# Optimization experiments

Hardware: AMD Instinct MI355X
Metric: run time of the kernel (lower is better)

The kernel has to match this reference:

```python
import jax, jax.numpy as jnp
import numpy as np

B, S, D, H = 8, 8192, 256, 256


def setup_inputs() -> dict:
    key = jax.random.key(0)
    ks = jax.random.split(key, 5)
    scale = 1.0 / np.sqrt(D)  # mimic nn.Linear init scale
    return {
        "x": jax.random.normal(ks[0], (B, S, D), dtype=jnp.float32),
        "h0": jnp.zeros((B, 1, H), dtype=jnp.float32),
        "w_h_w": jax.random.normal(ks[1], (H, D), dtype=jnp.float32) * scale,
        "w_h_b": jax.random.normal(ks[2], (H,), dtype=jnp.float32) * scale,
        "w_z_w": jax.random.normal(ks[3], (H, D), dtype=jnp.float32) * scale,
        "w_z_b": jax.random.normal(ks[4], (H,), dtype=jnp.float32) * scale,
    }


def reference(x, h0, w_h_w, w_h_b, w_z_w, w_z_b):
    # Projections over the whole sequence (same math as per-step Linear calls)
    z = jax.nn.sigmoid(jnp.einsum('bsd,hd->bsh', x, w_z_w) + w_z_b)  # [B,S,H]
    h_tilde = jnp.einsum('bsd,hd->bsh', x, w_h_w) + w_h_b            # [B,S,H]

    def step(h_prev, zh):
        z_t, ht_t = zh  # each [B,H]
        h_t = (1.0 - z_t) * h_prev + z_t * ht_t
        return h_t, h_t

    # scan over time axis; carry is [B,H]
    _, hs = jax.lax.scan(step, h0[:, 0],
                         (jnp.swapaxes(z, 0, 1), jnp.swapaxes(h_tilde, 0, 1)))
    return jnp.swapaxes(hs, 0, 1)  # [B,S,H]
```

## Files before the change

### kernel.cpp

```cpp
#include <hip/hip_runtime.h>
#include <math.h>


constexpr int B_ = 8;
constexpr int S_ = 8192;
constexpr int D_ = 256;
constexpr int H_ = 256;
constexpr int M_ = B_ * S_;
constexpr int CHUNKS = 128;
constexpr int CLEN = S_ / CHUNKS;

typedef __attribute__((ext_vector_type(8))) short bf16x8;
typedef __attribute__((ext_vector_type(4))) float f32x4;

__device__ __forceinline__ uint pack2bf(float f0, float f1) {
  const uint u0 = __float_as_uint(f0) + 0x8000u;
  const uint u1 = __float_as_uint(f1) + 0x8000u;
  return __builtin_amdgcn_perm(u1, u0, 0x07060302u);
}

__device__ __forceinline__ float a_of(uint u) { return __uint_as_float(u << 16); }
__device__ __forceinline__ float b_of(uint u) { return __uint_as_float(u & 0xFFFF0000u); }

__global__ __launch_bounds__(256) void gemm_zh(
    const float* __restrict__ x,
    const float* __restrict__ whw, const float* __restrict__ whb,
    const float* __restrict__ wzw, const float* __restrict__ wzb,
    uint* __restrict__ ab, float2* __restrict__ chunkPQ)
{
  __shared__ ushort xs[128][72];
  __shared__ ushort wzs[64][72];
  __shared__ ushort whs[64][72];

  const int tid = threadIdx.x;
  const int g    = blockIdx.x;
  const int xcd  = g & 7;
  const int loc  = g >> 3;
  const int nt   = loc & 3;
  const int panel = (loc >> 2) * 8 + xcd;
  const int m0 = panel * 128;
  const int n0 = nt * 64;

  const int lane = tid & 63;
  const int w  = tid >> 6;
  const int mb = (w & 1) * 64;
  const int nb = (w >> 1) * 32;
  const int q  = lane >> 4;
  const int cn = lane & 15;

  f32x4 accz[4][2] = {};
  f32x4 acch[4][2] = {};

  for (int k0 = 0; k0 < D_; k0 += 64) {
    __syncthreads();
#pragma unroll
    for (int f = 0; f < 8; f++) {
      const int idx = tid + 256 * f;
      const int row = idx >> 4, seg = idx & 15;
      float4 v = *(const float4*)(x + (size_t)(m0 + row) * D_ + k0 + seg * 4);
      *(uint2*)&xs[row][seg * 4] =
          make_uint2(pack2bf(v.x, v.y), pack2bf(v.z, v.w));
    }
#pragma unroll
    for (int f = 0; f < 4; f++) {
      const int idx = tid + 256 * f;
      const int row = idx >> 4, seg = idx & 15;
      float4 vz = *(const float4*)(wzw + (size_t)(n0 + row) * D_ + k0 + seg * 4);
      float4 vh = *(const float4*)(whw + (size_t)(n0 + row) * D_ + k0 + seg * 4);
      *(uint2*)&wzs[row][seg * 4] =
          make_uint2(pack2bf(vz.x, vz.y), pack2bf(vz.z, vz.w));
      *(uint2*)&whs[row][seg * 4] =
          make_uint2(pack2bf(vh.x, vh.y), pack2bf(vh.z, vh.w));
    }
    __syncthreads();
#pragma unroll
    for (int ks = 0; ks < 2; ks++) {
      const int kk = ks * 32 + q * 8;
      bf16x8 af[4], bz[2], bh[2];
#pragma unroll
      for (int i = 0; i < 4; i++)
        af[i] = *(const bf16x8*)&xs[mb + i * 16 + cn][kk];
#pragma unroll
      for (int j = 0; j < 2; j++) {
        bz[j] = *(const bf16x8*)&wzs[nb + j * 16 + cn][kk];
        bh[j] = *(const bf16x8*)&whs[nb + j * 16 + cn][kk];
      }
#pragma unroll
      for (int i = 0; i < 4; i++)
#pragma unroll
        for (int j = 0; j < 2; j++) {
          accz[i][j] = __builtin_amdgcn_mfma_f32_16x16x32_bf16(af[i], bz[j], accz[i][j], 0, 0, 0);
          acch[i][j] = __builtin_amdgcn_mfma_f32_16x16x32_bf16(af[i], bh[j], acch[i][j], 0, 0, 0);
        }
    }
  }

  const int row0 = m0 + mb;
  const int bb2  = row0 >> 13;
  const int cc   = (row0 & 8191) >> 6;

#pragma unroll
  for (int j = 0; j < 2; j++) {
    const int ch = n0 + nb + j * 16 + cn;
    const float zb = wzb[ch], hb = whb[ch];
    uint u[4][4];
#pragma unroll
    for (int i = 0; i < 4; i++) {
#pragma unroll
      for (int r = 0; r < 4; r++) {
        const int row = m0 + mb + i * 16 + q * 4 + r;
        const float zpre = accz[i][j][r] + zb;
        const float hpre = acch[i][j][r] + hb;
        const float e = __expf(-zpre);
        const float rcp = __builtin_amdgcn_rcpf(1.0f + e);
        const uint pk = pack2bf(e * rcp, hpre * rcp);
        ab[(size_t)row * H_ + ch] = pk;
        u[i][r] = pk;
      }
    }
    float P[4], Q[4];
#pragma unroll
    for (int i = 0; i < 4; i++) {
      float Pi = 1.f, Qi = 0.f;
#pragma unroll
      for (int r = 0; r < 4; r++) {
        const float a  = a_of(u[i][r]);
        const float bv = b_of(u[i][r]);
        Qi = fmaf(a, Qi, bv);
        Pi *= a;
      }
      P[i] = Pi; Q[i] = Qi;
    }
#pragma unroll
    for (int i = 0; i < 4; i++) {
      {
        const float Pp = __shfl_xor(P[i], 16);
        const float Qp = __shfl_xor(Q[i], 16);
        const bool later = (lane & 16) != 0;
        Q[i] = later ? fmaf(P[i], Qp, Q[i]) : fmaf(Pp, Q[i], Qp);
        P[i] = P[i] * Pp;
      }
      {
        const float Pp = __shfl_xor(P[i], 32);
        const float Qp = __shfl_xor(Q[i], 32);
        const bool later = (lane & 32) != 0;
        Q[i] = later ? fmaf(P[i], Qp, Q[i]) : fmaf(Pp, Q[i], Qp);
        P[i] = P[i] * Pp;
      }
    }
    float Pc = P[0], Qc = Q[0];
#pragma unroll
    for (int i = 1; i < 4; i++) {
      Qc = fmaf(P[i], Qc, Q[i]);
      Pc *= P[i];
    }
    if (lane < 16)
      chunkPQ[((size_t)bb2 * CHUNKS + cc) * H_ + ch] = make_float2(Pc, Qc);
  }
}

__global__ __launch_bounds__(256) void scan_phaseB(
    const float* __restrict__ h0in, const float2* __restrict__ pq,
    float* __restrict__ hstate)
{
  const int b = blockIdx.x;
  const int h = threadIdx.x;
  const size_t base = (size_t)b * CHUNKS * H_ + h;
  float hc = h0in[(size_t)b * H_ + h];
  for (int c0 = 0; c0 < CHUNKS; c0 += 16) {
    float2 v[16];
#pragma unroll
    for (int j = 0; j < 16; j++)
      v[j] = pq[base + (size_t)(c0 + j) * H_];
#pragma unroll
    for (int j = 0; j < 16; j++) {
      hstate[base + (size_t)(c0 + j) * H_] = hc;
      hc = fmaf(v[j].x, hc, v[j].y);
    }
  }
}

__global__ __launch_bounds__(256) void scan_phaseC(
    const uint* __restrict__ ab, const float* __restrict__ hstate,
    float* __restrict__ out)
{
  const int cid = blockIdx.x * 4 + (threadIdx.x >> 6);
  const int b = cid >> 7;
  const int c = cid & (CHUNKS - 1);
  const int ch4 = (threadIdx.x & 63) * 4;
  const size_t ebase = ((size_t)b * S_ + (size_t)c * CLEN) * H_ + ch4;

  float4 h4 = *(const float4*)(hstate + ((size_t)b * CHUNKS + c) * H_ + ch4);
  float h0v = h4.x, h1v = h4.y, h2v = h4.z, h3v = h4.w;

#pragma unroll
  for (int t0 = 0; t0 < CLEN; t0 += 8) {
    uint4 v[8];
#pragma unroll
    for (int j = 0; j < 8; j++)
      v[j] = *(const uint4*)(ab + ebase + (size_t)(t0 + j) * H_);
#pragma unroll
    for (int j = 0; j < 8; j++) {
      float4 o;
      o.x = h0v = fmaf(a_of(v[j].x), h0v, b_of(v[j].x));
      o.y = h1v = fmaf(a_of(v[j].y), h1v, b_of(v[j].y));
      o.z = h2v = fmaf(a_of(v[j].z), h2v, b_of(v[j].z));
      o.w = h3v = fmaf(a_of(v[j].w), h3v, b_of(v[j].w));
      *(float4*)(out + ebase + (size_t)(t0 + j) * H_) = o;
    }
  }
}

extern "C" void kernel_launch(void* const* d_in, const int* in_sizes, int n_in,
                              void* d_out, int out_size, void* d_ws, size_t ws_size,
                              hipStream_t stream) {
  const float* x   = (const float*)d_in[0];
  const float* h0  = (const float*)d_in[1];
  const float* whw = (const float*)d_in[2];
  const float* whb = (const float*)d_in[3];
  const float* wzw = (const float*)d_in[4];
  const float* wzb = (const float*)d_in[5];
  float* out = (float*)d_out;

  uint*   ab      = (uint*)d_ws;
  float2* chunkPQ = (float2*)(ab + (size_t)M_ * H_);
  float*  hstate  = (float*)(chunkPQ + (size_t)B_ * CHUNKS * H_);

  gemm_zh<<<(M_ / 128) * 4, 256, 0, stream>>>(x, whw, whb, wzw, wzb, ab, chunkPQ);
  scan_phaseB<<<B_, 256, 0, stream>>>(h0, (const float2*)chunkPQ, hstate);
  scan_phaseC<<<(B_ * CHUNKS) / 4, 256, 0, stream>>>(ab, hstate, out);
}
```

Measured before the change: 185.2 us.

## Pre-convert weights to bf16 once and widen GEMM tile to 128 columns

Adds a small prep kernel that converts both weight matrices to bf16 once, so the GEMM loads packed bf16 weights with 16-byte loads instead of converting fp32 weights in every block. The GEMM block grows to 512 threads covering a 128x128 output tile, halving the number of times each x panel is read and converted. The scan phase C is relaunched as one 64-thread block per chunk. This costs an extra kernel launch and more shared memory per block, which may reduce occupancy.

After: 177.2 us. 4.3% less time.

```diff
diff --git a/kernel.cpp b/kernel.cpp
--- a/kernel.cpp
+++ b/kernel.cpp
@@ -22,24 +22,34 @@
 __device__ __forceinline__ float a_of(uint u) { return __uint_as_float(u << 16); }
 __device__ __forceinline__ float b_of(uint u) { return __uint_as_float(u & 0xFFFF0000u); }
 
-__global__ __launch_bounds__(256) void gemm_zh(
-    const float* __restrict__ x,
-    const float* __restrict__ whw, const float* __restrict__ whb,
-    const float* __restrict__ wzw, const float* __restrict__ wzb,
+__global__ __launch_bounds__(256) void prep_w(
+    const float* __restrict__ wzw, const float* __restrict__ whw,
+    uint4* __restrict__ wb)
+{
+  const int u = blockIdx.x * 256 + threadIdx.x;
+  const int proj = u >> 13;
+  const float* s = (proj ? whw : wzw) + (size_t)(u & 8191) * 8;
+  wb[u] = make_uint4(pack2bf(s[0], s[1]), pack2bf(s[2], s[3]),
+                     pack2bf(s[4], s[5]), pack2bf(s[6], s[7]));
+}
+
+__global__ __launch_bounds__(512, 4) void gemm_zh(
+    const float* __restrict__ x, const ushort* __restrict__ wbu,
+    const float* __restrict__ whb, const float* __restrict__ wzb,
     uint* __restrict__ ab, float2* __restrict__ chunkPQ)
 {
   __shared__ ushort xs[128][72];
-  __shared__ ushort wzs[64][72];
-  __shared__ ushort whs[64][72];
+  __shared__ ushort wzs[128][72];
+  __shared__ ushort whs[128][72];
 
   const int tid = threadIdx.x;
   const int g    = blockIdx.x;
   const int xcd  = g & 7;
   const int loc  = g >> 3;
-  const int nt   = loc & 3;
-  const int panel = (loc >> 2) * 8 + xcd;
+  const int nt   = loc & 1;
+  const int panel = (loc >> 1) * 8 + xcd;
   const int m0 = panel * 128;
-  const int n0 = nt * 64;
+  const int n0 = nt * 128;
 
   const int lane = tid & 63;
   const int w  = tid >> 6;
@@ -54,8 +64,8 @@
   for (int k0 = 0; k0 < D_; k0 += 64) {
     __syncthreads();
 #pragma unroll
-    for (int f = 0; f < 8; f++) {
-      const int idx = tid + 256 * f;
+    for (int f = 0; f < 4; f++) {
+      const int idx = tid + 512 * f;
       const int row = idx >> 4, seg = idx & 15;
       float4 v = *(const float4*)(x + (size_t)(m0 + row) * D_ + k0 + seg * 4);
       *(uint2*)&xs[row][seg * 4] =
@@ -63,14 +73,13 @@
     }
 #pragma unroll
     for (int f = 0; f < 4; f++) {
-      const int idx = tid + 256 * f;
-      const int row = idx >> 4, seg = idx & 15;
-      float4 vz = *(const float4*)(wzw + (size_t)(n0 + row) * D_ + k0 + seg * 4);
-      float4 vh = *(const float4*)(whw + (size_t)(n0 + row) * D_ + k0 + seg * 4);
-      *(uint2*)&wzs[row][seg * 4] =
-          make_uint2(pack2bf(vz.x, vz.y), pack2bf(vz.z, vz.w));
-      *(uint2*)&whs[row][seg * 4] =
-          make_uint2(pack2bf(vh.x, vh.y), pack2bf(vh.z, vh.w));
+      const int idx = tid + 512 * f;
+      const int proj = idx >> 10;
+      const int r   = (idx >> 3) & 127, seg = idx & 7;
+      const uint4 v = *(const uint4*)(wbu + (size_t)proj * H_ * D_ +
+                                      (size_t)(n0 + r) * D_ + k0 + seg * 8);
+      ushort* dst = proj ? &whs[r][seg * 8] : &wzs[r][seg * 8];
+      *(uint4*)dst = v;
     }
     __syncthreads();
 #pragma unroll
@@ -180,14 +189,14 @@
   }
 }
 
-__global__ __launch_bounds__(256) void scan_phaseC(
+__global__ __launch_bounds__(64) void scan_phaseC(
     const uint* __restrict__ ab, const float* __restrict__ hstate,
     float* __restrict__ out)
 {
-  const int cid = blockIdx.x * 4 + (threadIdx.x >> 6);
+  const int cid = blockIdx.x;
   const int b = cid >> 7;
   const int c = cid & (CHUNKS - 1);
-  const int ch4 = (threadIdx.x & 63) * 4;
+  const int ch4 = threadIdx.x * 4;
   const size_t ebase = ((size_t)b * S_ + (size_t)c * CLEN) * H_ + ch4;
 
   float4 h4 = *(const float4*)(hstate + ((size_t)b * CHUNKS + c) * H_ + ch4);
@@ -225,8 +234,11 @@
   uint*   ab      = (uint*)d_ws;
   float2* chunkPQ = (float2*)(ab + (size_t)M_ * H_);
   float*  hstate  = (float*)(chunkPQ + (size_t)B_ * CHUNKS * H_);
-
-  gemm_zh<<<(M_ / 128) * 4, 256, 0, stream>>>(x, whw, whb, wzw, wzb, ab, chunkPQ);
+  ushort* wb      = (ushort*)(hstate + (size_t)B_ * CHUNKS * H_);
+
+  prep_w<<<64, 256, 0, stream>>>(wzw, whw, (uint4*)wb);
+  gemm_zh<<<(M_ / 128) * (H_ / 128), 512, 0, stream>>>(
+      x, wb, whb, wzb, ab, chunkPQ);
   scan_phaseB<<<B_, 256, 0, stream>>>(h0, (const float2*)chunkPQ, hstate);
-  scan_phaseC<<<(B_ * CHUNKS) / 4, 256, 0, stream>>>(ab, hstate, out);
-}
+  scan_phaseC<<<B_ * CHUNKS, 64, 0, stream>>>(ab, hstate, out);
+}
```
